# Performance work log

Hardware: AMD Instinct MI355X
Metric: run time of the kernel (lower is better)

## Reference

```python
import jax, jax.numpy as jnp
import numpy as np
from jax import lax

E = 16          # num_experts
CAP = 256       # capacity
MAX_IT = 3      # max_iterations
LPF = 2.0       # load_penalty_factor
DTEMP = 2.0     # diversity_temp
MIN_USAGE = 0.05
NC = 10         # num_classes
TC = 256        # trunk_channels
B = 2048
MIN_TOK = max(1, int(B * MIN_USAGE))        # 102
K_STATIC = min(B, max(CAP, MIN_TOK))        # static top-k width per expert claim


def setup_inputs() -> dict:
    key = jax.random.key(0)
    ks = jax.random.split(key, 16)
    d = {}
    d['x'] = jax.random.normal(ks[0], (B, 3, 32, 32), jnp.float32)
    chans = [(3, 32), (32, 64), (64, 128), (128, 256)]
    for i, (ci, co) in enumerate(chans, 1):
        d[f'cw{i}'] = jax.random.normal(ks[i], (co, ci, 3, 3), jnp.float32) * (1.0 / np.sqrt(ci * 9))
        d[f'cb{i}'] = jnp.zeros((co,), jnp.float32)
        d[f'g{i}'] = jnp.ones((co,), jnp.float32)
        d[f'be{i}'] = jnp.zeros((co,), jnp.float32)
        d[f'm{i}'] = jnp.zeros((co,), jnp.float32)
        d[f'v{i}'] = jnp.ones((co,), jnp.float32)
    d['gw1'] = jax.random.normal(ks[5], (E, TC, TC // 2), jnp.float32) * 0.05
    d['gb1'] = jnp.zeros((E, TC // 2), jnp.float32)
    d['gw2'] = jax.random.normal(ks[6], (E, TC // 2), jnp.float32) * 0.05
    d['gb2'] = jnp.zeros((E,), jnp.float32)
    d['cls_w'] = jax.random.normal(ks[7], (E, NC, TC), jnp.float32) * 0.01
    d['cls_b'] = jnp.zeros((E, NC), jnp.float32)
    d['usage_ema'] = jnp.ones((E,), jnp.float32) / E
    return d


def _conv_bn_relu(x, w, b, g, beta, m, v):
    y = lax.conv_general_dilated(x, w, (1, 1), 'SAME', dimension_numbers=('NCHW', 'OIHW', 'NCHW'))
    y = y + b[None, :, None, None]
    scale = (g / jnp.sqrt(v + 1e-5))[None, :, None, None]
    return jax.nn.relu((y - m[None, :, None, None]) * scale + beta[None, :, None, None])


def _maxpool2(x):
    return lax.reduce_window(x, -jnp.inf, lax.max, (1, 1, 2, 2), (1, 1, 2, 2), 'VALID')


def _forward(x, cw1, cb1, g1, be1, m1, v1, cw2, cb2, g2, be2, m2, v2,
             cw3, cb3, g3, be3, m3, v3, cw4, cb4, g4, be4, m4, v4,
             gw1, gb1, gw2, gb2, cls_w, cls_b, usage_ema):
    # trunk (eval-mode BN)
    h = _conv_bn_relu(x, cw1, cb1, g1, be1, m1, v1)
    h = _conv_bn_relu(h, cw2, cb2, g2, be2, m2, v2)
    h = _maxpool2(h)
    h = _conv_bn_relu(h, cw3, cb3, g3, be3, m3, v3)
    h = _conv_bn_relu(h, cw4, cb4, g4, be4, m4, v4)
    h = _maxpool2(h)
    feats = h.mean(axis=(2, 3))  # AdaptiveAvgPool2d(1)+Flatten -> [B, TC]

    # per-expert classifier heads
    logits_e = jnp.einsum('bd,ecd->bec', feats, cls_w) + cls_b[None]  # [B,E,NC]
    probs = jax.nn.softmax(logits_e, axis=2)
    ent = -(probs * jnp.log(jnp.clip(probs, 1e-12))).sum(axis=2)      # [B,E]
    confidence = -ent

    # per-expert gates (vectorized over experts); dropout is identity in eval
    hidden = jax.nn.relu(jnp.einsum('bd,edh->beh', feats, gw1) + gb1[None])
    expert_scores = (jnp.einsum('beh,eh->be', hidden, gw2) + gb2[None]) / DTEMP

    routing_scores = 0.6 * expert_scores + 0.4 * confidence - LPF * usage_ema[None]

    # iterative capacity-constrained routing (eval: expert order 0..E-1)
    D = jnp.zeros((B, E), bool)
    loads = jnp.zeros((E,), jnp.float32)
    avail = jnp.ones((B,), bool)
    ranks = jnp.arange(K_STATIC)
    for it in range(MAX_IT):
        # penalty from loads at the START of the iteration
        pscores = routing_scores - (it + 1) * LPF * loads[None]
        for j in range(E):
            sj = jnp.where(avail, pscores[:, j], -jnp.inf)
            vc = avail.sum().astype(jnp.int32)
            rc = jnp.maximum(0, CAP - loads[j].astype(jnp.int32))
            ntc = jnp.where((rc == 0) | (vc == 0), 0,
                            jnp.maximum(jnp.minimum(rc, vc), jnp.minimum(MIN_TOK, vc)))
            _, idx = lax.top_k(sj, K_STATIC)
            take = ranks < ntc
            claimed = jnp.zeros((B,), bool).at[idx].set(take)
            D = D.at[:, j].set(D[:, j] | claimed)
            avail = avail & ~claimed
            loads = loads.at[j].add(ntc.astype(jnp.float32))

    # fallback: sequentially assign leftover tokens to least-loaded of top-3
    def fb(carry, inp):
        Dc, lc = carry
        sc, av, i = inp
        _, t3 = lax.top_k(sc, 3)
        best = t3[jnp.argmin(lc[t3])]
        Dc = Dc.at[i, best].set(Dc[i, best] | av)
        lc = lc.at[best].add(av.astype(jnp.float32))
        return (Dc, lc), None

    (D, loads), _ = lax.scan(fb, (D, loads), (routing_scores, avail, jnp.arange(B)))

    Df = D.astype(jnp.float32)
    active = routing_scores * Df
    active = active - active.max(axis=1, keepdims=True)
    weights = jax.nn.softmax(active + (Df - 1.0) * 1e9, axis=1)
    final_logits = (weights[:, :, None] * logits_e).sum(axis=1)
    return final_logits, routing_scores, D


def reference(x, cw1, cb1, g1, be1, m1, v1, cw2, cb2, g2, be2, m2, v2,
              cw3, cb3, g3, be3, m3, v3, cw4, cb4, g4, be4, m4, v4,
              gw1, gb1, gw2, gb2, cls_w, cls_b, usage_ema):
    return _forward(x, cw1, cb1, g1, be1, m1, v1, cw2, cb2, g2, be2, m2, v2,
                    cw3, cb3, g3, be3, m3, v3, cw4, cb4, g4, be4, m4, v4,
                    gw1, gb1, gw2, gb2, cls_w, cls_b, usage_ema)
```

## Files before the change

### kernel.cpp

```cpp
#include <hip/hip_runtime.h>

typedef __attribute__((ext_vector_type(8))) short short8;
typedef __attribute__((ext_vector_type(4))) float f32x4;

__device__ __forceinline__ unsigned short f2bf(float f) {
  unsigned u = __float_as_uint(f);
  unsigned r = (u + 0x7fffu + ((u >> 16) & 1u)) >> 16;
  return (unsigned short)r;
}
__device__ __forceinline__ float bf2f(unsigned short h) {
  return __uint_as_float(((unsigned)h) << 16);
}

__global__ __launch_bounds__(256) void bnprep_kernel(
    const float* __restrict__ g, const float* __restrict__ be,
    const float* __restrict__ m, const float* __restrict__ v,
    const float* __restrict__ b, float* __restrict__ A, float* __restrict__ C, int n)
{
  int i = blockIdx.x * 256 + threadIdx.x;
  if (i < n) {
    float s = g[i] / sqrtf(v[i] + 1e-5f);
    A[i] = s;
    C[i] = (b[i] - m[i]) * s + be[i];
  }
}

__global__ __launch_bounds__(256) void wprep2_kernel(
    const float* __restrict__ w, unsigned short* __restrict__ wPk, int CO, int CI)
{
  int NCB = CI / 32, NF = CO / 16;
  int total = 9 * NCB * NF * 64;
  int idx = blockIdx.x * 256 + threadIdx.x;
  if (idx >= total) return;
  int lane = idx & 63;
  int unit = idx >> 6;
  int f = unit % NF;
  int cb = (unit / NF) % NCB;
  int s = unit / (NF * NCB);
  int co = f * 16 + (lane & 15);
  int ci0 = cb * 32 + (lane >> 4) * 8;
  long base = (long)unit * 1024 + lane * 8;
  #pragma unroll
  for (int j = 0; j < 8; ++j) {
    float v = w[((long)co * CI + ci0 + j) * 9 + s];
    unsigned short h = f2bf(v);
    unsigned short l = f2bf(v - bf2f(h));
    wPk[base + j] = h;
    wPk[base + 512 + j] = l;
  }
}

__global__ __launch_bounds__(512, 2) void conv12_kernel(
    const float* __restrict__ xin, const float* __restrict__ cw1,
    const float* __restrict__ A1p, const float* __restrict__ C1p,
    const unsigned short* __restrict__ wPk, const float* __restrict__ Ap,
    const float* __restrict__ Cp, unsigned short* __restrict__ outA)
{
  constexpr int TY = 16, TX = 32;
  constexpr int PXW = TX + 2;
  constexpr int PXT = (TY + 2) * PXW;
  constexpr int PLSTR = PXT * 8 + 8;
  constexpr int NF = 4;
  __shared__ alignas(16) unsigned short smem[8 * PLSTR];
  __shared__ alignas(16) float sx[2160];
  __shared__ alignas(16) float sw[864];

  const int nwg = gridDim.x;
  const int orig = blockIdx.x;
  const int q = nwg >> 3, r = nwg & 7;
  const int xcd = orig & 7, pos = orig >> 3;
  const int bx = (xcd < r ? xcd * (q + 1) : r * (q + 1) + (xcd - r) * q) + pos;

  const int img = bx >> 1;
  const int tY0 = (bx & 1) * 16;

  const int tid = threadIdx.x;
  const int lane = tid & 63;
  const int lx = lane & 15, kg = lane >> 4;
  const int w = tid >> 6;

  for (int i = tid; i < 2160; i += 512) {
    int c = i / 720, rem = i - c * 720;
    int yy = rem / 36, xx2 = rem - yy * 36;
    int gy = tY0 + yy - 2, gx = xx2 - 2;
    sx[i] = (gy >= 0 && gy < 32 && gx >= 0 && gx < 32)
            ? xin[(long)img * 3072 + c * 1024 + gy * 32 + gx] : 0.f;
  }
  for (int i = tid; i < 864; i += 512) {
    int co = i & 31, kk = i >> 5;
    sw[kk * 32 + co] = cw1[(long)co * 27 + kk];
  }
  __syncthreads();

  #pragma unroll 1
  for (int p = 0; p < 2; ++p) {
    int px = p * 512 + tid;
    if (px < PXT) {
      int ry = px / PXW, rx = px - ry * PXW;
      int gy = tY0 + ry - 1, gx = rx - 1;
      if (gy >= 0 && gy < 32 && gx >= 0 && gx < 32) {
        #pragma unroll 1
        for (int half = 0; half < 2; ++half) {
          float acc[16];
          #pragma unroll
          for (int j = 0; j < 16; ++j) acc[j] = 0.f;
          #pragma unroll
          for (int c = 0; c < 3; ++c) {
            #pragma unroll
            for (int k = 0; k < 9; ++k) {
              int dy = k / 3, dx = k - 3 * (k / 3);
              float iv = sx[c * 720 + (ry + dy) * 36 + rx + dx];
              const float4* w4 = (const float4*)(sw + (c * 9 + k) * 32 + half * 16);
              #pragma unroll
              for (int q2 = 0; q2 < 4; ++q2) {
                float4 wv = w4[q2];
                acc[4 * q2 + 0] += iv * wv.x; acc[4 * q2 + 1] += iv * wv.y;
                acc[4 * q2 + 2] += iv * wv.z; acc[4 * q2 + 3] += iv * wv.w;
              }
            }
          }
          #pragma unroll
          for (int j2 = 0; j2 < 2; ++j2) {
            short8 hv, lv;
            #pragma unroll
            for (int j = 0; j < 8; ++j) {
              int co = half * 16 + j2 * 8 + j;
              float vv = fmaxf(acc[j2 * 8 + j] * A1p[co] + C1p[co], 0.f);
              unsigned short h = f2bf(vv);
              hv[j] = (short)h;
              lv[j] = (short)f2bf(vv - bf2f(h));
            }
            int plane = half * 2 + j2;
            *(short8*)(smem + plane * PLSTR + px * 8) = hv;
            *(short8*)(smem + (plane + 4) * PLSTR + px * 8) = lv;
          }
        }
      } else {
        short8 zz = {0, 0, 0, 0, 0, 0, 0, 0};
        #pragma unroll
        for (int cc = 0; cc < 8; ++cc)
          *(short8*)(smem + cc * PLSTR + px * 8) = zz;
      }
    }
  }
  __syncthreads();

  f32x4 acc[4][4];
  #pragma unroll
  for (int i = 0; i < 4; ++i)
    #pragma unroll
    for (int j = 0; j < 4; ++j) acc[i][j] = (f32x4){0.f, 0.f, 0.f, 0.f};

  for (int s = 0; s < 9; ++s) {
    const int ky = s / 3, kx = s - 3 * (s / 3);
    const long ub = ((long)(s * NF)) * 1024 + lane * 8;
    short8 bh[4], bl[4];
    #pragma unroll
    for (int nf = 0; nf < 4; ++nf) {
      bh[nf] = *(const short8*)(wPk + ub + nf * 1024);
      bl[nf] = *(const short8*)(wPk + ub + nf * 1024 + 512);
    }
    #pragma unroll
    for (int mf = 0; mf < 4; ++mf) {
      const int yoff = mf >> 1;
      const int xb = (mf & 1) * 16;
      const int y = w * 2 + yoff;
      const int pxa = (y + ky) * PXW + xb + kx + lx;
      short8 ah = *(const short8*)(smem + kg * PLSTR + pxa * 8);
      short8 al = *(const short8*)(smem + (kg + 4) * PLSTR + pxa * 8);
      #pragma unroll
      for (int nf = 0; nf < 4; ++nf)
        acc[mf][nf] = __builtin_amdgcn_mfma_f32_16x16x32_bf16(ah, bh[nf], acc[mf][nf], 0, 0, 0);
      #pragma unroll
      for (int nf = 0; nf < 4; ++nf)
        acc[mf][nf] = __builtin_amdgcn_mfma_f32_16x16x32_bf16(ah, bl[nf], acc[mf][nf], 0, 0, 0);
      #pragma unroll
      for (int nf = 0; nf < 4; ++nf)
        acc[mf][nf] = __builtin_amdgcn_mfma_f32_16x16x32_bf16(al, bh[nf], acc[mf][nf], 0, 0, 0);
    }
  }
  __syncthreads();

  float Ar[4], Cr[4];
  #pragma unroll
  for (int nf = 0; nf < 4; ++nf) {
    int co = nf * 16 + lx;
    Ar[nf] = Ap[co]; Cr[nf] = Cp[co];
  }

  unsigned short* slice = smem + w * 2048;
  const int py = (tY0 >> 1) + w;
  #pragma unroll
  for (int xf = 0; xf < 2; ++xf) {
    #pragma unroll
    for (int rp = 0; rp < 2; ++rp) {
      int ox = xf * 8 + 2 * kg + rp;
      #pragma unroll
      for (int nf = 0; nf < 4; ++nf) {
        float v0 = fmaxf(fmaxf(acc[xf][nf][2 * rp], acc[xf][nf][2 * rp + 1]),
                         fmaxf(acc[xf + 2][nf][2 * rp], acc[xf + 2][nf][2 * rp + 1]));
        float vv = fmaxf(v0 * Ar[nf] + Cr[nf], 0.f);
        unsigned short h = f2bf(vv);
        unsigned short l = f2bf(vv - bf2f(h));
        slice[(ox * 2 + 0) * 64 + nf * 16 + lx] = h;
        slice[(ox * 2 + 1) * 64 + nf * 16 + lx] = l;
      }
    }
  }
  #pragma unroll
  for (int v = 0; v < 4; ++v) {
    int hoff = lane * 8 + v * 512;
    int x2 = hoff >> 7, rem = hoff & 127;
    int seg = rem >> 6, inner = rem & 63;
    short8 d = *(const short8*)(slice + hoff);
    *(short8*)(outA + ((long)img * 256 + py * 16 + x2) * 128 + seg * 64 + inner) = d;
  }
}

__global__ __launch_bounds__(512, 1) void convmf45_kernel(
    const unsigned short* __restrict__ act2,
    const unsigned short* __restrict__ wPk3, const float* __restrict__ A3p,
    const float* __restrict__ C3p,
    const unsigned short* __restrict__ wPk4, const float* __restrict__ A4p,
    const float* __restrict__ C4p, float* __restrict__ feats)
{
  constexpr int PLSTR3 = 2056;
  constexpr int ZOFF = 32 * PLSTR3;
  constexpr int PXW2 = 18, PXT2 = 324;
  constexpr int PLSTR2 = PXT2 * 8 + 8;
  __shared__ alignas(16) unsigned short smem[ZOFF + 64];

  const int nwg = gridDim.x;
  const int orig = blockIdx.x;
  const int q = nwg >> 3, r = nwg & 7;
  const int xcd = orig & 7, pos = orig >> 3;
  const int img = (xcd < r ? xcd * (q + 1) : r * (q + 1) + (xcd - r) * q) + pos;

  const int tid = threadIdx.x;
  const int lane = tid & 63;
  const int lx = lane & 15, kg = lane >> 4;
  const int w = tid >> 6;

  if (tid < 8) {
    short8 zz = {0, 0, 0, 0, 0, 0, 0, 0};
    *(short8*)(smem + ZOFF + tid * 8) = zz;
  }

  f32x4 acc3[2][8];
  #pragma unroll
  for (int i = 0; i < 2; ++i)
    #pragma unroll
    for (int j = 0; j < 8; ++j) acc3[i][j] = (f32x4){0.f, 0.f, 0.f, 0.f};

  for (int cb = 0; cb < 2; ++cb) {
    __syncthreads();
    for (int t2 = tid; t2 < PXT2 * 8; t2 += 512) {
      int px = t2 >> 3, c = t2 & 7;
      int ry = px / PXW2, rx = px - ry * PXW2;
      int gy = ry - 1, gx = rx - 1;
      float4 v = (float4){0.f, 0.f, 0.f, 0.f};
      if (gy >= 0 && gy < 16 && gx >= 0 && gx < 16) {
        int coff = (c < 4) ? (cb * 32 + c * 8) : (64 + cb * 32 + (c - 4) * 8);
        v = *(const float4*)(act2 + ((long)img * 256 + gy * 16 + gx) * 128 + coff);
      }
      *(float4*)(smem + c * PLSTR2 + px * 8) = v;
    }
    __syncthreads();

    for (int s = 0; s < 9; ++s) {
      const int ky = s / 3, kx = s - 3 * (s / 3);
      short8 ah[2], al[2];
      #pragma unroll
      for (int mf = 0; mf < 2; ++mf) {
        const int pxa = (w * 2 + mf + ky) * PXW2 + kx + lx;
        ah[mf] = *(const short8*)(smem + kg * PLSTR2 + pxa * 8);
        al[mf] = *(const short8*)(smem + (kg + 4) * PLSTR2 + pxa * 8);
      }
      const long ub = ((long)(s * 2 + cb) * 8) * 1024 + lane * 8;
      {
        short8 bh[4], bl[4];
        #pragma unroll
        for (int nf = 0; nf < 4; ++nf) {
          bh[nf] = *(const short8*)(wPk3 + ub + nf * 1024);
          bl[nf] = *(const short8*)(wPk3 + ub + nf * 1024 + 512);
        }
        #pragma unroll
        for (int mf = 0; mf < 2; ++mf) {
          #pragma unroll
          for (int nf = 0; nf < 4; ++nf)
            acc3[mf][nf] = __builtin_amdgcn_mfma_f32_16x16x32_bf16(ah[mf], bh[nf], acc3[mf][nf], 0, 0, 0);
          #pragma unroll
          for (int nf = 0; nf < 4; ++nf)
            acc3[mf][nf] = __builtin_amdgcn_mfma_f32_16x16x32_bf16(ah[mf], bl[nf], acc3[mf][nf], 0, 0, 0);
          #pragma unroll
          for (int nf = 0; nf < 4; ++nf)
            acc3[mf][nf] = __builtin_amdgcn_mfma_f32_16x16x32_bf16(al[mf], bh[nf], acc3[mf][nf], 0, 0, 0);
        }
      }
      {
        short8 bh[4], bl[4];
        #pragma unroll
        for (int nf = 0; nf < 4; ++nf) {
          bh[nf] = *(const short8*)(wPk3 + ub + (4 + nf) * 1024);
          bl[nf] = *(const short8*)(wPk3 + ub + (4 + nf) * 1024 + 512);
        }
        #pragma unroll
        for (int mf = 0; mf < 2; ++mf) {
          #pragma unroll
          for (int nf = 0; nf < 4; ++nf)
            acc3[mf][4 + nf] = __builtin_amdgcn_mfma_f32_16x16x32_bf16(ah[mf], bh[nf], acc3[mf][4 + nf], 0, 0, 0);
          #pragma unroll
          for (int nf = 0; nf < 4; ++nf)
            acc3[mf][4 + nf] = __builtin_amdgcn_mfma_f32_16x16x32_bf16(ah[mf], bl[nf], acc3[mf][4 + nf], 0, 0, 0);
          #pragma unroll
          for (int nf = 0; nf < 4; ++nf)
            acc3[mf][4 + nf] = __builtin_amdgcn_mfma_f32_16x16x32_bf16(al[mf], bh[nf], acc3[mf][4 + nf], 0, 0, 0);
        }
      }
    }
  }
  __syncthreads();

  #pragma unroll
  for (int mf = 0; mf < 2; ++mf) {
    int y = w * 2 + mf;
    #pragma unroll
    for (int rr = 0; rr < 4; ++rr) {
      int px = y * 16 + 4 * kg + rr;
      #pragma unroll
      for (int nf = 0; nf < 8; ++nf) {
        int co = nf * 16 + lx;
        float vv = fmaxf(acc3[mf][nf][rr] * A3p[co] + C3p[co], 0.f);
        unsigned short h = f2bf(vv);
        unsigned short l = f2bf(vv - bf2f(h));
        int plane = co >> 3, j = co & 7;
        smem[plane * PLSTR3 + px * 8 + j] = h;
        smem[(plane + 16) * PLSTR3 + px * 8 + j] = l;
      }
    }
  }
  __syncthreads();

  const int pxg = w >> 1;
  const int cog = w & 1;

  f32x4 acc[4][8];
  #pragma unroll
  for (int i = 0; i < 4; ++i)
    #pragma unroll
    for (int j = 0; j < 8; ++j) acc[i][j] = (f32x4){0.f, 0.f, 0.f, 0.f};

  for (int cb = 0; cb < 4; ++cb) {
    for (int s = 0; s < 9; ++s) {
      const int ky = s / 3, kx = s - 3 * (s / 3);
      short8 ah[4], al[4];
      #pragma unroll
      for (int mf = 0; mf < 4; ++mf) {
        int gy = pxg * 4 + mf + ky - 1;
        int gxx = lx + kx - 1;
        bool ok = (gy >= 0) && (gy < 16) && (gxx >= 0) && (gxx < 16);
        int pxo = (gy * 16 + gxx) * 8;
        int offH = ok ? ((cb * 4 + kg) * PLSTR3 + pxo) : ZOFF;
        int offL = ok ? ((16 + cb * 4 + kg) * PLSTR3 + pxo) : ZOFF;
        ah[mf] = *(const short8*)(smem + offH);
        al[mf] = *(const short8*)(smem + offL);
      }
      const long ub = ((long)(s * 4 + cb) * 16 + cog * 8) * 1024 + lane * 8;
      {
        short8 bh[4], bl[4];
        #pragma unroll
        for (int nf = 0; nf < 4; ++nf) {
          bh[nf] = *(const short8*)(wPk4 + ub + nf * 1024);
          bl[nf] = *(const short8*)(wPk4 + ub + nf * 1024 + 512);
        }
        #pragma unroll
        for (int mf = 0; mf < 4; ++mf) {
          #pragma unroll
          for (int nf = 0; nf < 4; ++nf)
            acc[mf][nf] = __builtin_amdgcn_mfma_f32_16x16x32_bf16(ah[mf], bh[nf], acc[mf][nf], 0, 0, 0);
          #pragma unroll
          for (int nf = 0; nf < 4; ++nf)
            acc[mf][nf] = __builtin_amdgcn_mfma_f32_16x16x32_bf16(ah[mf], bl[nf], acc[mf][nf], 0, 0, 0);
          #pragma unroll
          for (int nf = 0; nf < 4; ++nf)
            acc[mf][nf] = __builtin_amdgcn_mfma_f32_16x16x32_bf16(al[mf], bh[nf], acc[mf][nf], 0, 0, 0);
        }
      }
      {
        short8 bh[4], bl[4];
        #pragma unroll
        for (int nf = 0; nf < 4; ++nf) {
          bh[nf] = *(const short8*)(wPk4 + ub + (4 + nf) * 1024);
          bl[nf] = *(const short8*)(wPk4 + ub + (4 + nf) * 1024 + 512);
        }
        #pragma unroll
        for (int mf = 0; mf < 4; ++mf) {
          #pragma unroll
          for (int nf = 0; nf < 4; ++nf)
            acc[mf][4 + nf] = __builtin_amdgcn_mfma_f32_16x16x32_bf16(ah[mf], bh[nf], acc[mf][4 + nf], 0, 0, 0);
          #pragma unroll
          for (int nf = 0; nf < 4; ++nf)
            acc[mf][4 + nf] = __builtin_amdgcn_mfma_f32_16x16x32_bf16(ah[mf], bl[nf], acc[mf][4 + nf], 0, 0, 0);
          #pragma unroll
          for (int nf = 0; nf < 4; ++nf)
            acc[mf][4 + nf] = __builtin_amdgcn_mfma_f32_16x16x32_bf16(al[mf], bh[nf], acc[mf][4 + nf], 0, 0, 0);
        }
      }
    }
  }
  __syncthreads();

  float psum[8];
  #pragma unroll
  for (int j = 0; j < 8; ++j) psum[j] = 0.f;
  #pragma unroll
  for (int j = 0; j < 8; ++j) {
    int co = (cog * 8 + j) * 16 + lx;
    float Ar = A4p[co], Cr = C4p[co];
    #pragma unroll
    for (int u = 0; u < 2; ++u) {
      #pragma unroll
      for (int v = 0; v < 2; ++v) {
        float vm = fmaxf(fmaxf(acc[2 * u][j][2 * v], acc[2 * u][j][2 * v + 1]),
                         fmaxf(acc[2 * u + 1][j][2 * v], acc[2 * u + 1][j][2 * v + 1]));
        psum[j] += fmaxf(vm * Ar + Cr, 0.f);
      }
    }
  }
  #pragma unroll
  for (int j = 0; j < 8; ++j) {
    psum[j] += __shfl_xor(psum[j], 16);
    psum[j] += __shfl_xor(psum[j], 32);
  }
  float* sR = (float*)smem;
  if (kg == 0) {
    #pragma unroll
    for (int j = 0; j < 8; ++j) sR[w * 128 + j * 16 + lx] = psum[j];
  }
  __syncthreads();
  if (tid < 256) {
    int cogT = tid >> 7, cl = tid & 127;
    float s = 0.f;
    #pragma unroll
    for (int p = 0; p < 4; ++p) s += sR[(p * 2 + cogT) * 128 + cl];
    feats[(long)img * 256 + tid] = s * (1.f / 64.f);
  }
}

__global__ __launch_bounds__(256) void heads2_kernel(
    const float* __restrict__ feats, const float* __restrict__ gw1,
    const float* __restrict__ gb1, const float* __restrict__ gw2,
    const float* __restrict__ gb2, const float* __restrict__ clsw,
    const float* __restrict__ clsb, const float* __restrict__ usage,
    float* __restrict__ logits_e, float* __restrict__ rs_out)
{
  __shared__ float sF[64 * 257];
  __shared__ float sLg[4 * 64 * 10];
  __shared__ float sRed[4 * 64];
  const int tid = threadIdx.x;
  const int b0 = blockIdx.x * 64;
  const int e  = blockIdx.y;

  for (int idx = tid; idx < 64 * 64; idx += 256) {
    int t = idx >> 6, dg = idx & 63;
    float4 v = ((const float4*)(feats + (long)(b0 + t) * 256))[dg];
    float* p = sF + t * 257 + dg * 4;
    p[0] = v.x; p[1] = v.y; p[2] = v.z; p[3] = v.w;
  }
  __syncthreads();

  const int t  = tid & 63;
  const int hw = __builtin_amdgcn_readfirstlane(tid >> 6);

  {
    float acc[10];
    #pragma unroll
    for (int c = 0; c < 10; ++c) acc[c] = 0.f;
    const float* fp = sF + t * 257 + hw * 64;
    const float* cw = clsw + (long)e * 2560 + hw * 64;
    for (int dd = 0; dd < 64; ++dd) {
      float f = fp[dd];
      #pragma unroll
      for (int c = 0; c < 10; ++c) acc[c] += f * cw[c * 256 + dd];
    }
    #pragma unroll
    for (int c = 0; c < 10; ++c) sLg[(hw * 64 + t) * 10 + c] = acc[c];
  }
  {
    float gacc[32];
    #pragma unroll
    for (int j = 0; j < 32; ++j) gacc[j] = 0.f;
    const float* wb = gw1 + ((long)e * 256) * 128 + hw * 32;
    const float* fp = sF + t * 257;
    for (int d = 0; d < 256; ++d) {
      float f = fp[d];
      const float4* w4 = (const float4*)(wb + (long)d * 128);
      #pragma unroll
      for (int qq = 0; qq < 8; ++qq) {
        float4 wv = w4[qq];
        gacc[4 * qq + 0] += f * wv.x; gacc[4 * qq + 1] += f * wv.y;
        gacc[4 * qq + 2] += f * wv.z; gacc[4 * qq + 3] += f * wv.w;
      }
    }
    float s = 0.f;
    const float* b1 = gb1 + e * 128 + hw * 32;
    const float* w2 = gw2 + e * 128 + hw * 32;
    #pragma unroll
    for (int j = 0; j < 32; ++j) s += fmaxf(gacc[j] + b1[j], 0.f) * w2[j];
    sRed[hw * 64 + t] = s;
  }
  __syncthreads();

  if (tid < 64) {
    float es = (sRed[t] + sRed[64 + t] + sRed[128 + t] + sRed[192 + t] + gb2[e]) * 0.5f;
    float lg[10];
    #pragma unroll
    for (int c = 0; c < 10; ++c)
      lg[c] = sLg[t * 10 + c] + sLg[(64 + t) * 10 + c]
            + sLg[(128 + t) * 10 + c] + sLg[(192 + t) * 10 + c] + clsb[e * 10 + c];
    float mx = lg[0];
    #pragma unroll
    for (int c = 1; c < 10; ++c) mx = fmaxf(mx, lg[c]);
    float S = 0.f, ps[10];
    #pragma unroll
    for (int c = 0; c < 10; ++c) { ps[c] = expf(lg[c] - mx); S += ps[c]; }
    float inv = 1.f / S, ent = 0.f;
    #pragma unroll
    for (int c = 0; c < 10; ++c) { float p = ps[c] * inv; ent -= p * logf(fmaxf(p, 1e-12f)); }
    float rsv = 0.6f * es + 0.4f * (-ent) - 2.0f * usage[e];
    rs_out[(long)(b0 + t) * 16 + e] = rsv;
    #pragma unroll
    for (int c = 0; c < 10; ++c)
      logits_e[((long)(b0 + t) * 16 + e) * 10 + c] = lg[c];
  }
}

__global__ __launch_bounds__(1024) void sort_kernel(
    const float* __restrict__ rs, unsigned* __restrict__ sortedIdx)
{
  __shared__ unsigned long long sk[2048];
  const int e = blockIdx.x;
  const unsigned tid = threadIdx.x;
  for (int i = tid; i < 2048; i += 1024) {
    float f = rs[(long)i * 16 + e];
    unsigned u = __float_as_uint(f);
    u ^= (u >> 31) ? 0xFFFFFFFFu : 0x80000000u;
    sk[i] = ((unsigned long long)(~u) << 32) | (unsigned)i;
  }
  for (unsigned k = 2; k <= 2048; k <<= 1) {
    for (unsigned j = k >> 1; j > 0; j >>= 1) {
      __syncthreads();
      unsigned i = ((tid & ~(j - 1)) << 1) | (tid & (j - 1));
      unsigned p = i | j;
      bool asc = ((i & k) == 0);
      unsigned long long a = sk[i], b = sk[p];
      if ((a > b) == asc) { sk[i] = b; sk[p] = a; }
    }
  }
  __syncthreads();
  for (int i = tid; i < 2048; i += 1024)
    sortedIdx[(long)e * 2048 + i] = (unsigned)(sk[i] & 0xFFFFFFFFull);
}

__global__ __launch_bounds__(64) void routing2_kernel(
    const unsigned* __restrict__ sortedIdx, const float* __restrict__ rs,
    unsigned* __restrict__ dmaskOut)
{
  __shared__ unsigned char sAvail[2048];
  __shared__ unsigned sDm[2048];
  __shared__ int sLoads[16];
  const int lane = threadIdx.x;
  for (int i = lane; i < 2048; i += 64) { sAvail[i] = 1; sDm[i] = 0; }
  if (lane < 16) sLoads[lane] = 0;
  __syncthreads();

  int vc = 2048;
  for (int it = 0; it < 3; ++it) {
    for (int j = 0; j < 16; ++j) {
      int lj = sLoads[j];
      int rc = 256 - lj; if (rc < 0) rc = 0;
      int ntc = 0;
      if (rc > 0 && vc > 0) {
        int a = rc < vc ? rc : vc;
        int b2 = vc < 102 ? vc : 102;
        ntc = a > b2 ? a : b2;
      }
      if (ntc > 0) {
        const unsigned* se = sortedIdx + (long)j * 2048;
        int taken = 0;
        for (int base = 0; base < 2048; base += 64) {
          if (taken >= ntc) break;
          unsigned tok = se[base + lane];
          int fl = sAvail[tok] ? 1 : 0;
          unsigned long long bm = __ballot(fl);
          int pre = taken + __popcll(bm & ((1ull << lane) - 1ull));
          if (fl && pre < ntc) { sAvail[tok] = 0; sDm[tok] |= (1u << j); }
          taken += (int)__popcll(bm);
          __syncthreads();
        }
        if (lane == 0) sLoads[j] = lj + ntc;
        vc -= ntc;
        __syncthreads();
      }
    }
  }

  if (vc > 0) {
    if (lane == 0) {
      for (int i = 0; i < 2048; ++i) {
        if (!sAvail[i]) continue;
        float s0 = -3.4e38f, s1 = s0, s2 = s0; int e0 = 0, e1 = 0, e2 = 0;
        for (int e = 0; e < 16; ++e) {
          float s = rs[i * 16 + e];
          if (s > s0)      { s2 = s1; e2 = e1; s1 = s0; e1 = e0; s0 = s; e0 = e; }
          else if (s > s1) { s2 = s1; e2 = e1; s1 = s;  e1 = e; }
          else if (s > s2) { s2 = s;  e2 = e; }
        }
        int best = e0, bl = sLoads[e0];
        if (sLoads[e1] < bl) { best = e1; bl = sLoads[e1]; }
        if (sLoads[e2] < bl) { best = e2; bl = sLoads[e2]; }
        sDm[i] |= (1u << best);
        sLoads[best] += 1;
      }
    }
    __syncthreads();
  }

  for (int i = lane; i < 2048; i += 64) dmaskOut[i] = sDm[i];
}

__global__ __launch_bounds__(256) void combine_kernel(
    const unsigned* __restrict__ dmask, const float* __restrict__ rs,
    const float* __restrict__ L, float* __restrict__ out, float* __restrict__ Dout)
{
  int i = blockIdx.x * 256 + threadIdx.x;
  if (i >= 2048) return;
  unsigned dm = dmask[i];
  float r[16];
  #pragma unroll
  for (int e = 0; e < 16; ++e) r[e] = rs[i * 16 + e];
  float mx = -3.4e38f;
  #pragma unroll
  for (int e = 0; e < 16; ++e) {
    float v = ((dm >> e) & 1u) ? r[e] : 0.0f;
    mx = fmaxf(mx, v);
  }
  float w[16], S = 0.f;
  #pragma unroll
  for (int e = 0; e < 16; ++e) {
    w[e] = ((dm >> e) & 1u) ? expf(r[e] - mx) : 0.0f;
    S += w[e];
  }
  float inv = 1.f / S;
  #pragma unroll
  for (int c = 0; c < 10; ++c) {
    float a = 0.f;
    #pragma unroll
    for (int e = 0; e < 16; ++e) a += w[e] * L[((long)i * 16 + e) * 10 + c];
    out[i * 10 + c] = a * inv;
  }
  #pragma unroll
  for (int e = 0; e < 16; ++e)
    Dout[(long)i * 16 + e] = ((dm >> e) & 1u) ? 1.0f : 0.0f;
}

extern "C" void kernel_launch(void* const* d_in, const int* in_sizes, int n_in,
                              void* d_out, int out_size, void* d_ws, size_t ws_size,
                              hipStream_t stream)
{
  const float* x    = (const float*)d_in[0];
  const float* cw1  = (const float*)d_in[1];
  const float* cb1  = (const float*)d_in[2];
  const float* g1   = (const float*)d_in[3];
  const float* be1  = (const float*)d_in[4];
  const float* m1   = (const float*)d_in[5];
  const float* v1   = (const float*)d_in[6];
  const float* cw2  = (const float*)d_in[7];
  const float* cb2  = (const float*)d_in[8];
  const float* g2   = (const float*)d_in[9];
  const float* be2  = (const float*)d_in[10];
  const float* m2   = (const float*)d_in[11];
  const float* v2   = (const float*)d_in[12];
  const float* cw3  = (const float*)d_in[13];
  const float* cb3  = (const float*)d_in[14];
  const float* g3   = (const float*)d_in[15];
  const float* be3  = (const float*)d_in[16];
  const float* m3   = (const float*)d_in[17];
  const float* v3   = (const float*)d_in[18];
  const float* cw4  = (const float*)d_in[19];
  const float* cb4  = (const float*)d_in[20];
  const float* g4   = (const float*)d_in[21];
  const float* be4  = (const float*)d_in[22];
  const float* m4   = (const float*)d_in[23];
  const float* v4   = (const float*)d_in[24];
  const float* gw1  = (const float*)d_in[25];
  const float* gb1  = (const float*)d_in[26];
  const float* gw2  = (const float*)d_in[27];
  const float* gb2  = (const float*)d_in[28];
  const float* clsw = (const float*)d_in[29];
  const float* clsb = (const float*)d_in[30];
  const float* usage = (const float*)d_in[31];

  float* out = (float*)d_out;
  float* ws  = (float*)d_ws;

  float* A1 = ws + 0;   float* C1 = ws + 32;
  float* A2 = ws + 64;  float* C2 = ws + 128;
  float* A3 = ws + 192; float* C3 = ws + 320;
  float* A4 = ws + 448; float* C4 = ws + 704;
  float* feats   = ws + 1024;
  float* logitsE = ws + 525312;
  unsigned* sortedIdx = (unsigned*)(ws + 852992);
  unsigned* dmask     = (unsigned*)(ws + 885760);
  unsigned short* wPk2 = (unsigned short*)(ws + 887808);
  unsigned short* wPk3 = (unsigned short*)(ws + 906240);
  unsigned short* wPk4 = (unsigned short*)(ws + 979968);
  const long bufBase = 1274880;

  long wsFloats = (long)(ws_size / 4);
  long availF = wsFloats - bufBase;
  long chunkL = availF / 16384;
  int chunk = (int)(chunkL < 1 ? 1 : (chunkL > 2048 ? 2048 : chunkL));

  bnprep_kernel<<<1, 256, 0, stream>>>(g1, be1, m1, v1, cb1, A1, C1, 32);
  bnprep_kernel<<<1, 256, 0, stream>>>(g2, be2, m2, v2, cb2, A2, C2, 64);
  bnprep_kernel<<<1, 256, 0, stream>>>(g3, be3, m3, v3, cb3, A3, C3, 128);
  bnprep_kernel<<<1, 256, 0, stream>>>(g4, be4, m4, v4, cb4, A4, C4, 256);
  wprep2_kernel<<<(2304 + 255) / 256, 256, 0, stream>>>(cw2, wPk2, 64, 32);
  wprep2_kernel<<<(9216 + 255) / 256, 256, 0, stream>>>(cw3, wPk3, 128, 64);
  wprep2_kernel<<<(36864 + 255) / 256, 256, 0, stream>>>(cw4, wPk4, 256, 128);

  unsigned short* act2buf = (unsigned short*)(ws + bufBase);

  for (int ib = 0; ib < 2048; ib += chunk) {
    int n = 2048 - ib; if (n > chunk) n = chunk;
    conv12_kernel<<<dim3(n * 2), 512, 0, stream>>>(
        x + (long)ib * 3072, cw1, A1, C1, wPk2, A2, C2, act2buf);
    convmf45_kernel<<<dim3(n), 512, 0, stream>>>(
        act2buf, wPk3, A3, C3, wPk4, A4, C4, feats + (long)ib * 256);
  }

  float* rsOut = out + 20480;
  heads2_kernel<<<dim3(32, 16), 256, 0, stream>>>(feats, gw1, gb1, gw2, gb2,
                                                  clsw, clsb, usage, logitsE, rsOut);
  sort_kernel<<<16, 1024, 0, stream>>>(rsOut, sortedIdx);
  routing2_kernel<<<1, 64, 0, stream>>>(sortedIdx, rsOut, dmask);
  combine_kernel<<<8, 256, 0, stream>>>(dmask, rsOut, logitsE, out, out + 53248);
}
```

Before: 1.212 ms.

## Software-pipeline weight fragment loads and double-buffer conv3 input staging

```diff
diff --git a/kernel.cpp b/kernel.cpp
--- a/kernel.cpp
+++ b/kernel.cpp
@@ -228,6 +228,7 @@
   constexpr int ZOFF = 32 * PLSTR3;
   constexpr int PXW2 = 18, PXT2 = 324;
   constexpr int PLSTR2 = PXT2 * 8 + 8;
+  constexpr int SBUF = 8 * PLSTR2;
   __shared__ alignas(16) unsigned short smem[ZOFF + 64];
 
   const int nwg = gridDim.x;
@@ -252,70 +253,101 @@
     #pragma unroll
     for (int j = 0; j < 8; ++j) acc3[i][j] = (f32x4){0.f, 0.f, 0.f, 0.f};
 
-  for (int cb = 0; cb < 2; ++cb) {
-    __syncthreads();
-    for (int t2 = tid; t2 < PXT2 * 8; t2 += 512) {
-      int px = t2 >> 3, c = t2 & 7;
-      int ry = px / PXW2, rx = px - ry * PXW2;
-      int gy = ry - 1, gx = rx - 1;
-      float4 v = (float4){0.f, 0.f, 0.f, 0.f};
-      if (gy >= 0 && gy < 16 && gx >= 0 && gx < 16) {
-        int coff = (c < 4) ? (cb * 32 + c * 8) : (64 + cb * 32 + (c - 4) * 8);
-        v = *(const float4*)(act2 + ((long)img * 256 + gy * 16 + gx) * 128 + coff);
-      }
-      *(float4*)(smem + c * PLSTR2 + px * 8) = v;
-    }
-    __syncthreads();
-
-    for (int s = 0; s < 9; ++s) {
-      const int ky = s / 3, kx = s - 3 * (s / 3);
-      short8 ah[2], al[2];
-      #pragma unroll
-      for (int mf = 0; mf < 2; ++mf) {
-        const int pxa = (w * 2 + mf + ky) * PXW2 + kx + lx;
-        ah[mf] = *(const short8*)(smem + kg * PLSTR2 + pxa * 8);
-        al[mf] = *(const short8*)(smem + (kg + 4) * PLSTR2 + pxa * 8);
-      }
-      const long ub = ((long)(s * 2 + cb) * 8) * 1024 + lane * 8;
-      {
-        short8 bh[4], bl[4];
+  float4 av[6];
+  #define LOADA2(CB)                                                         \
+    _Pragma("unroll")                                                        \
+    for (int i = 0; i < 6; ++i) {                                            \
+      int idx = tid + i * 512;                                               \
+      if (idx < PXT2 * 8) {                                                  \
+        int px = idx >> 3, c = idx & 7;                                      \
+        int ry = px / PXW2, rx = px - ry * PXW2;                             \
+        int gy = ry - 1, gx = rx - 1;                                        \
+        float4 v = (float4){0.f, 0.f, 0.f, 0.f};                             \
+        if (gy >= 0 && gy < 16 && gx >= 0 && gx < 16) {                      \
+          int coff = (c < 4) ? ((CB) * 32 + c * 8) : (64 + (CB) * 32 + (c - 4) * 8); \
+          v = *(const float4*)(act2 + ((long)img * 256 + gy * 16 + gx) * 128 + coff); \
+        }                                                                    \
+        av[i] = v;                                                           \
+      }                                                                      \
+    }
+  #define WRITEA2(BUF)                                                       \
+    _Pragma("unroll")                                                        \
+    for (int i = 0; i < 6; ++i) {                                            \
+      int idx = tid + i * 512;                                               \
+      if (idx < PXT2 * 8) {                                                  \
+        int px = idx >> 3, c = idx & 7;                                      \
+        *(float4*)(smem + (BUF) * SBUF + c * PLSTR2 + px * 8) = av[i];       \
+      }                                                                      \
+    }
+
+  LOADA2(0); WRITEA2(0);
+  __syncthreads();
+  LOADA2(1);
+
+  {
+    short8 p3h[4], p3l[4];
+    long ub = (long)lane * 8;
+    #pragma unroll
+    for (int nf = 0; nf < 4; ++nf) {
+      p3h[nf] = *(const short8*)(wPk3 + ub + nf * 1024);
+      p3l[nf] = *(const short8*)(wPk3 + ub + nf * 1024 + 512);
+    }
+    #pragma unroll 1
+    for (int cb = 0; cb < 2; ++cb) {
+      const unsigned short* sbase = smem + cb * SBUF;
+      #pragma unroll 1
+      for (int s = 0; s < 9; ++s) {
+        const int ky = s / 3, kx = s - 3 * (s / 3);
+        short8 ah[2], al[2];
+        #pragma unroll
+        for (int mf = 0; mf < 2; ++mf) {
+          const int pxa = (w * 2 + mf + ky) * PXW2 + kx + lx;
+          ah[mf] = *(const short8*)(sbase + kg * PLSTR2 + pxa * 8);
+          al[mf] = *(const short8*)(sbase + (kg + 4) * PLSTR2 + pxa * 8);
+        }
+        short8 c1h[4], c1l[4];
         #pragma unroll
         for (int nf = 0; nf < 4; ++nf) {
-          bh[nf] = *(const short8*)(wPk3 + ub + nf * 1024);
-          bl[nf] = *(const short8*)(wPk3 + ub + nf * 1024 + 512);
+          c1h[nf] = *(const short8*)(wPk3 + ub + (4 + nf) * 1024);
+          c1l[nf] = *(const short8*)(wPk3 + ub + (4 + nf) * 1024 + 512);
         }
         #pragma unroll
         for (int mf = 0; mf < 2; ++mf) {
           #pragma unroll
           for (int nf = 0; nf < 4; ++nf)
-            acc3[mf][nf] = __builtin_amdgcn_mfma_f32_16x16x32_bf16(ah[mf], bh[nf], acc3[mf][nf], 0, 0, 0);
-          #pragma unroll
-          for (int nf = 0; nf < 4; ++nf)
-            acc3[mf][nf] = __builtin_amdgcn_mfma_f32_16x16x32_bf16(ah[mf], bl[nf], acc3[mf][nf], 0, 0, 0);
-          #pragma unroll
-          for (int nf = 0; nf < 4; ++nf)
-            acc3[mf][nf] = __builtin_amdgcn_mfma_f32_16x16x32_bf16(al[mf], bh[nf], acc3[mf][nf], 0, 0, 0);
-        }
-      }
-      {
-        short8 bh[4], bl[4];
-        #pragma unroll
-        for (int nf = 0; nf < 4; ++nf) {
-          bh[nf] = *(const short8*)(wPk3 + ub + (4 + nf) * 1024);
-          bl[nf] = *(const short8*)(wPk3 + ub + (4 + nf) * 1024 + 512);
-        }
+            acc3[mf][nf] = __builtin_amdgcn_mfma_f32_16x16x32_bf16(ah[mf], p3h[nf], acc3[mf][nf], 0, 0, 0);
+          #pragma unroll
+          for (int nf = 0; nf < 4; ++nf)
+            acc3[mf][nf] = __builtin_amdgcn_mfma_f32_16x16x32_bf16(ah[mf], p3l[nf], acc3[mf][nf], 0, 0, 0);
+          #pragma unroll
+          for (int nf = 0; nf < 4; ++nf)
+            acc3[mf][nf] = __builtin_amdgcn_mfma_f32_16x16x32_bf16(al[mf], p3h[nf], acc3[mf][nf], 0, 0, 0);
+        }
+        long ubn = (s < 8) ? (ub + 16384) : (ub - 122880);
+        if (!(cb == 1 && s == 8)) {
+          #pragma unroll
+          for (int nf = 0; nf < 4; ++nf) {
+            p3h[nf] = *(const short8*)(wPk3 + ubn + nf * 1024);
+            p3l[nf] = *(const short8*)(wPk3 + ubn + nf * 1024 + 512);
+          }
+        }
+        ub = ubn;
         #pragma unroll
         for (int mf = 0; mf < 2; ++mf) {
           #pragma unroll
           for (int nf = 0; nf < 4; ++nf)
-            acc3[mf][4 + nf] = __builtin_amdgcn_mfma_f32_16x16x32_bf16(ah[mf], bh[nf], acc3[mf][4 + nf], 0, 0, 0);
-          #pragma unroll
-          for (int nf = 0; nf < 4; ++nf)
-            acc3[mf][4 + nf] = __builtin_amdgcn_mfma_f32_16x16x32_bf16(ah[mf], bl[nf], acc3[mf][4 + nf], 0, 0, 0);
-          #pragma unroll
-          for (int nf = 0; nf < 4; ++nf)
-            acc3[mf][4 + nf] = __builtin_amdgcn_mfma_f32_16x16x32_bf16(al[mf], bh[nf], acc3[mf][4 + nf], 0, 0, 0);
-        }
+            acc3[mf][4 + nf] = __builtin_amdgcn_mfma_f32_16x16x32_bf16(ah[mf], c1h[nf], acc3[mf][4 + nf], 0, 0, 0);
+          #pragma unroll
+          for (int nf = 0; nf < 4; ++nf)
+            acc3[mf][4 + nf] = __builtin_amdgcn_mfma_f32_16x16x32_bf16(ah[mf], c1l[nf], acc3[mf][4 + nf], 0, 0, 0);
+          #pragma unroll
+          for (int nf = 0; nf < 4; ++nf)
+            acc3[mf][4 + nf] = __builtin_amdgcn_mfma_f32_16x16x32_bf16(al[mf], c1h[nf], acc3[mf][4 + nf], 0, 0, 0);
+        }
+      }
+      if (cb == 0) {
+        WRITEA2(1);
+        __syncthreads();
       }
     }
   }
@@ -350,60 +382,69 @@
     #pragma unroll
     for (int j = 0; j < 8; ++j) acc[i][j] = (f32x4){0.f, 0.f, 0.f, 0.f};
 
-  for (int cb = 0; cb < 4; ++cb) {
-    for (int s = 0; s < 9; ++s) {
-      const int ky = s / 3, kx = s - 3 * (s / 3);
-      short8 ah[4], al[4];
-      #pragma unroll
-      for (int mf = 0; mf < 4; ++mf) {
-        int gy = pxg * 4 + mf + ky - 1;
-        int gxx = lx + kx - 1;
-        bool ok = (gy >= 0) && (gy < 16) && (gxx >= 0) && (gxx < 16);
-        int pxo = (gy * 16 + gxx) * 8;
-        int offH = ok ? ((cb * 4 + kg) * PLSTR3 + pxo) : ZOFF;
-        int offL = ok ? ((16 + cb * 4 + kg) * PLSTR3 + pxo) : ZOFF;
-        ah[mf] = *(const short8*)(smem + offH);
-        al[mf] = *(const short8*)(smem + offL);
-      }
-      const long ub = ((long)(s * 4 + cb) * 16 + cog * 8) * 1024 + lane * 8;
-      {
-        short8 bh[4], bl[4];
+  {
+    short8 p4h[4], p4l[4];
+    long ub = ((long)cog * 8) * 1024 + lane * 8;
+    #pragma unroll
+    for (int nf = 0; nf < 4; ++nf) {
+      p4h[nf] = *(const short8*)(wPk4 + ub + nf * 1024);
+      p4l[nf] = *(const short8*)(wPk4 + ub + nf * 1024 + 512);
+    }
+    #pragma unroll 1
+    for (int cb = 0; cb < 4; ++cb) {
+      #pragma unroll 1
+      for (int s = 0; s < 9; ++s) {
+        const int ky = s / 3, kx = s - 3 * (s / 3);
+        short8 ah[4], al[4];
+        #pragma unroll
+        for (int mf = 0; mf < 4; ++mf) {
+          int gy = pxg * 4 + mf + ky - 1;
+          int gxx = lx + kx - 1;
+          bool ok = (gy >= 0) && (gy < 16) && (gxx >= 0) && (gxx < 16);
+          int pxo = (gy * 16 + gxx) * 8;
+          int offH = ok ? ((cb * 4 + kg) * PLSTR3 + pxo) : ZOFF;
+          int offL = ok ? ((16 + cb * 4 + kg) * PLSTR3 + pxo) : ZOFF;
+          ah[mf] = *(const short8*)(smem + offH);
+          al[mf] = *(const short8*)(smem + offL);
+        }
+        short8 c1h[4], c1l[4];
         #pragma unroll
         for (int nf = 0; nf < 4; ++nf) {
-          bh[nf] = *(const short8*)(wPk4 + ub + nf * 1024);
-          bl[nf] = *(const short8*)(wPk4 + ub + nf * 1024 + 512);
+          c1h[nf] = *(const short8*)(wPk4 + ub + (4 + nf) * 1024);
+          c1l[nf] = *(const short8*)(wPk4 + ub + (4 + nf) * 1024 + 512);
         }
         #pragma unroll
         for (int mf = 0; mf < 4; ++mf) {
           #pragma unroll
           for (int nf = 0; nf < 4; ++nf)
-            acc[mf][nf] = __builtin_amdgcn_mfma_f32_16x16x32_bf16(ah[mf], bh[nf], acc[mf][nf], 0, 0, 0);
-          #pragma unroll
-          for (int nf = 0; nf < 4; ++nf)
-            acc[mf][nf] = __builtin_amdgcn_mfma_f32_16x16x32_bf16(ah[mf], bl[nf], acc[mf][nf], 0, 0, 0);
-          #pragma unroll
-          for (int nf = 0; nf < 4; ++nf)
-            acc[mf][nf] = __builtin_amdgcn_mfma_f32_16x16x32_bf16(al[mf], bh[nf], acc[mf][nf], 0, 0, 0);
-        }
-      }
-      {
-        short8 bh[4], bl[4];
-        #pragma unroll
-        for (int nf = 0; nf < 4; ++nf) {
-          bh[nf] = *(const short8*)(wPk4 + ub + (4 + nf) * 1024);
-          bl[nf] = *(const short8*)(wPk4 + ub + (4 + nf) * 1024 + 512);
-        }
+            acc[mf][nf] = __builtin_amdgcn_mfma_f32_16x16x32_bf16(ah[mf], p4h[nf], acc[mf][nf], 0, 0, 0);
+          #pragma unroll
+          for (int nf = 0; nf < 4; ++nf)
+            acc[mf][nf] = __builtin_amdgcn_mfma_f32_16x16x32_bf16(ah[mf], p4l[nf], acc[mf][nf], 0, 0, 0);
+          #pragma unroll
+          for (int nf = 0; nf < 4; ++nf)
+            acc[mf][nf] = __builtin_amdgcn_mfma_f32_16x16x32_bf16(al[mf], p4h[nf], acc[mf][nf], 0, 0, 0);
+        }
+        long ubn = (s < 8) ? (ub + 65536) : (ub - 507904);
+        if (!(cb == 3 && s == 8)) {
+          #pragma unroll
+          for (int nf = 0; nf < 4; ++nf) {
+            p4h[nf] = *(const short8*)(wPk4 + ubn + nf * 1024);
+            p4l[nf] = *(const short8*)(wPk4 + ubn + nf * 1024 + 512);
+          }
+        }
+        ub = ubn;
         #pragma unroll
         for (int mf = 0; mf < 4; ++mf) {
           #pragma unroll
           for (int nf = 0; nf < 4; ++nf)
-            acc[mf][4 + nf] = __builtin_amdgcn_mfma_f32_16x16x32_bf16(ah[mf], bh[nf], acc[mf][4 + nf], 0, 0, 0);
-          #pragma unroll
-          for (int nf = 0; nf < 4; ++nf)
-            acc[mf][4 + nf] = __builtin_amdgcn_mfma_f32_16x16x32_bf16(ah[mf], bl[nf], acc[mf][4 + nf], 0, 0, 0);
-          #pragma unroll
-          for (int nf = 0; nf < 4; ++nf)
-            acc[mf][4 + nf] = __builtin_amdgcn_mfma_f32_16x16x32_bf16(al[mf], bh[nf], acc[mf][4 + nf], 0, 0, 0);
+            acc[mf][4 + nf] = __builtin_amdgcn_mfma_f32_16x16x32_bf16(ah[mf], c1h[nf], acc[mf][4 + nf], 0, 0, 0);
+          #pragma unroll
+          for (int nf = 0; nf < 4; ++nf)
+            acc[mf][4 + nf] = __builtin_amdgcn_mfma_f32_16x16x32_bf16(ah[mf], c1l[nf], acc[mf][4 + nf], 0, 0, 0);
+          #pragma unroll
+          for (int nf = 0; nf < 4; ++nf)
+            acc[mf][4 + nf] = __builtin_amdgcn_mfma_f32_16x16x32_bf16(al[mf], c1h[nf], acc[mf][4 + nf], 0, 0, 0);
         }
       }
     }
@@ -445,6 +486,8 @@
     for (int p = 0; p < 4; ++p) s += sR[(p * 2 + cogT) * 128 + cl];
     feats[(long)img * 256 + tid] = s * (1.f / 64.f);
   }
+  #undef LOADA2
+  #undef WRITEA2
 }
 
 __global__ __launch_bounds__(256) void heads2_kernel(
```

After: 1.203 ms. No clear change (-0.8%).
